# Kernel optimization log

Hardware: AMD Instinct MI355X
Metric: run time of the kernel (lower is better)

The kernel has to match this reference:

```python
import jax, jax.numpy as jnp
import numpy as np
import math

D = 1024
H = 16
HD = D // H
P = 64  # bias_proj_dim
B, N, M = 4, 1024, 2048
EPS_LN = 1e-5
EPS_NORM = 1e-12


def _ln(x, g, b):
    mu = jnp.mean(x, axis=-1, keepdims=True)
    var = jnp.var(x, axis=-1, keepdims=True)
    return (x - mu) * jax.lax.rsqrt(var + EPS_LN) * g + b


def _l2norm_dim1(x):
    # torch F.normalize(x, p=2) default dim=1 -> normalize over the sequence axis
    n = jnp.sqrt(jnp.sum(x * x, axis=1, keepdims=True))
    return x / jnp.maximum(n, EPS_NORM)


def setup_inputs() -> dict:
    key = jax.random.key(0)
    ks = jax.random.split(key, 16)
    s = 1.0 / math.sqrt(D)
    inp = {
        'dataset_features': jax.random.normal(ks[0], (B, N, D), jnp.float32),
        'visual_features': jax.random.normal(ks[1], (B, M, D), jnp.float32),
        # linear weights stored as (in, out): y = x @ W + b
        'wq_w': jax.random.normal(ks[2], (D, D), jnp.float32) * s,
        'wq_b': jnp.zeros((D,), jnp.float32),
        'wk_w': jax.random.normal(ks[3], (D, D), jnp.float32) * s,
        'wk_b': jnp.zeros((D,), jnp.float32),
        'wv_w': jax.random.normal(ks[4], (D, D), jnp.float32) * s,
        'wv_b': jnp.zeros((D,), jnp.float32),
        'wo_w': jax.random.normal(ks[5], (D, D), jnp.float32) * s,
        'wo_b': jnp.zeros((D,), jnp.float32),
        'gq_w': jax.random.normal(ks[6], (D, P), jnp.float32) * s,
        'gq_b': jnp.zeros((P,), jnp.float32),
        'gk_w': jax.random.normal(ks[7], (D, P), jnp.float32) * s,
        'gk_b': jnp.zeros((P,), jnp.float32),
        'pos_scale': jnp.asarray(2.0, jnp.float32),
        'neg_scale': jnp.asarray(50.0, jnp.float32),
        'attn_logit_scale': jnp.asarray(math.log(10.0), jnp.float32),
        'ln_q_g': jnp.ones((D,), jnp.float32),
        'ln_q_b': jnp.zeros((D,), jnp.float32),
        'ln_kv_g': jnp.ones((D,), jnp.float32),
        'ln_kv_b': jnp.zeros((D,), jnp.float32),
        'ln_out_g': jnp.ones((D,), jnp.float32),
        'ln_out_b': jnp.zeros((D,), jnp.float32),
        'ff1_w': jax.random.normal(ks[8], (D, 2 * D), jnp.float32) * s,
        'ff1_b': jnp.zeros((2 * D,), jnp.float32),
        'ff2_w': jax.random.normal(ks[9], (2 * D, D), jnp.float32) * (1.0 / math.sqrt(2 * D)),
        'ff2_b': jnp.zeros((D,), jnp.float32),
    }
    return inp


def reference(dataset_features, visual_features, wq_w, wq_b, wk_w, wk_b, wv_w, wv_b,
              wo_w, wo_b, gq_w, gq_b, gk_w, gk_b, pos_scale, neg_scale,
              attn_logit_scale, ln_q_g, ln_q_b, ln_kv_g, ln_kv_b, ln_out_g, ln_out_b,
              ff1_w, ff1_b, ff2_w, ff2_b):
    residual = dataset_features
    q_in = _ln(dataset_features, ln_q_g, ln_q_b)   # [B,N,D]
    kv_in = _ln(visual_features, ln_kv_g, ln_kv_b)  # [B,M,D]

    geo_q = _l2norm_dim1(q_in @ gq_w + gq_b)   # [B,N,P], normalized over N
    geo_k = _l2norm_dim1(kv_in @ gk_w + gk_b)  # [B,M,P], normalized over M
    bias_raw = jnp.einsum('bnp,bmp->bnm', geo_q, geo_k)  # [B,N,M]
    full_bias = jax.nn.relu(bias_raw) * pos_scale - jax.nn.relu(-bias_raw) * neg_scale

    q = (q_in @ wq_w + wq_b).reshape(B, N, H, HD).transpose(0, 2, 1, 3)   # [B,H,N,hd]
    k = (kv_in @ wk_w + wk_b).reshape(B, M, H, HD).transpose(0, 2, 1, 3)  # [B,H,M,hd]
    v = (kv_in @ wv_w + wv_b).reshape(B, M, H, HD).transpose(0, 2, 1, 3)

    logits = jnp.einsum('bhnd,bhmd->bhnm', q, k) / math.sqrt(HD)
    logits = logits * jnp.exp(attn_logit_scale)
    scores = logits + full_bias[:, None, :, :]
    attn = jax.nn.softmax(scores, axis=-1)
    out = jnp.einsum('bhnm,bhmd->bhnd', attn, v).transpose(0, 2, 1, 3).reshape(B, N, D)
    out = out @ wo_w + wo_b
    out = residual + out

    residual = out
    h = _ln(out, ln_out_g, ln_out_b)
    ff = jax.nn.gelu(h @ ff1_w + ff1_b, approximate=False) @ ff2_w + ff2_b
    return residual + ff
```

## Files before the change

kernel.cpp:

```cpp
#include <hip/hip_runtime.h>


typedef __bf16 bf16x8 __attribute__((ext_vector_type(8)));
typedef float  f32x4  __attribute__((ext_vector_type(4)));

__device__ inline f32x4 mfma16(bf16x8 a, bf16x8 b, f32x4 c) {
  return __builtin_amdgcn_mfma_f32_16x16x32_bf16(a, b, c, 0, 0, 0);
}

__device__ inline void glds16(const void* g, void* l) {
  __builtin_amdgcn_global_load_lds(
      (const __attribute__((address_space(1))) void*)g,
      (__attribute__((address_space(3))) void*)l, 16, 0, 0);
}

#define DB 1024
#define DH 16
#define DHD 64
#define DP 64
#define NB 4
#define NN 1024
#define NM 2048

__global__ __launch_bounds__(256) void k_transpose_all(
    const float* __restrict__ w0, const float* __restrict__ w1,
    const float* __restrict__ w2, const float* __restrict__ w3,
    const float* __restrict__ f1, const float* __restrict__ f2,
    const float* __restrict__ g0, const float* __restrict__ g1,
    __bf16* __restrict__ o0, __bf16* __restrict__ o1,
    __bf16* __restrict__ o2, __bf16* __restrict__ o3,
    __bf16* __restrict__ of1, __bf16* __restrict__ of2,
    __bf16* __restrict__ og0, __bf16* __restrict__ og1) {
  __shared__ float tile[32][33];
  int id = blockIdx.x;
  const float* in;
  __bf16* out;
  int K, O, x, y;
  if (id < 4096) {
    int mi = id >> 10, r = id & 1023;
    in = mi == 0 ? w0 : mi == 1 ? w1 : mi == 2 ? w2 : w3;
    out = mi == 0 ? o0 : mi == 1 ? o1 : mi == 2 ? o2 : o3;
    K = 1024; O = 1024; x = r & 31; y = r >> 5;
  } else if (id < 6144) {
    int r = id - 4096; in = f1; out = of1; K = 1024; O = 2048; x = r & 63; y = r >> 6;
  } else if (id < 8192) {
    int r = id - 6144; in = f2; out = of2; K = 2048; O = 1024; x = r & 31; y = r >> 5;
  } else if (id < 8256) {
    int r = id - 8192; in = g0; out = og0; K = 1024; O = 64; x = r & 1; y = r >> 1;
  } else {
    int r = id - 8256; in = g1; out = og1; K = 1024; O = 64; x = r & 1; y = r >> 1;
  }
  int k0 = y * 32, o0c = x * 32;
  int tx = threadIdx.x & 31, ty = threadIdx.x >> 5;
#pragma unroll
  for (int r = ty; r < 32; r += 8)
    tile[r][tx] = in[(size_t)(k0 + r) * O + (o0c + tx)];
  __syncthreads();
#pragma unroll
  for (int r = ty; r < 32; r += 8)
    out[(size_t)(o0c + r) * K + (k0 + tx)] = (__bf16)tile[tx][r];
}

__device__ inline void ln_body(const float* __restrict__ x,
                               const float* __restrict__ g,
                               const float* __restrict__ bb,
                               __bf16* __restrict__ y, size_t row) {
  int t = threadIdx.x;
  float4 v = ((const float4*)(x + row * 1024))[t];
  float s = v.x + v.y + v.z + v.w;
  float ss = v.x * v.x + v.y * v.y + v.z * v.z + v.w * v.w;
#pragma unroll
  for (int o = 32; o; o >>= 1) {
    s += __shfl_down(s, o, 64);
    ss += __shfl_down(ss, o, 64);
  }
  __shared__ float r1[4], r2[4];
  if ((t & 63) == 0) { r1[t >> 6] = s; r2[t >> 6] = ss; }
  __syncthreads();
  s = r1[0] + r1[1] + r1[2] + r1[3];
  ss = r2[0] + r2[1] + r2[2] + r2[3];
  float mu = s * (1.f / 1024.f);
  float rstd = rsqrtf(ss * (1.f / 1024.f) - mu * mu + 1e-5f);
  float4 gv = ((const float4*)g)[t];
  float4 bv = ((const float4*)bb)[t];
  __bf16* yr = y + row * 1024 + t * 4;
  yr[0] = (__bf16)((v.x - mu) * rstd * gv.x + bv.x);
  yr[1] = (__bf16)((v.y - mu) * rstd * gv.y + bv.y);
  yr[2] = (__bf16)((v.z - mu) * rstd * gv.z + bv.z);
  yr[3] = (__bf16)((v.w - mu) * rstd * gv.w + bv.w);
}

__global__ __launch_bounds__(256) void k_layernorm(
    const float* __restrict__ x, const float* __restrict__ g,
    const float* __restrict__ bb, __bf16* __restrict__ y) {
  ln_body(x, g, bb, y, blockIdx.x);
}

__global__ __launch_bounds__(256) void k_layernorm2(
    const float* __restrict__ x1, const float* __restrict__ g1,
    const float* __restrict__ b1, __bf16* __restrict__ y1,
    const float* __restrict__ x2, const float* __restrict__ g2,
    const float* __restrict__ b2, __bf16* __restrict__ y2) {
  int row = blockIdx.x;
  if (row < 4096) ln_body(x1, g1, b1, y1, row);
  else ln_body(x2, g2, b2, y2, row - 4096);
}

__global__ __launch_bounds__(256) void k_geo(
    const __bf16* __restrict__ qin, const __bf16* __restrict__ kvin,
    const __bf16* __restrict__ gqw, const __bf16* __restrict__ gkw,
    const float* __restrict__ gqb, const float* __restrict__ gkb,
    __bf16* __restrict__ geoq, __bf16* __restrict__ geok) {
  const int blk = blockIdx.x;
  const bool isq = blk < 128;
  const __bf16* A = isq ? qin : kvin;
  const __bf16* Bt = isq ? gqw : gkw;
  const float* bias = isq ? gqb : gkb;
  __bf16* C = isq ? geoq : geok;
  const int row0 = (isq ? blk : blk - 128) * 32;
  __shared__ __align__(16) __bf16 As[32][72], Bs[64][72];
  const int t = threadIdx.x, lane = t & 63, w = t >> 6;
  const int quad = lane >> 4, l15 = lane & 15;
  const int wr = w >> 1, wc = w & 1;
  const int sr = t >> 3, skc = (t & 7) * 8;
  const __bf16* aP = A + (size_t)(row0 + sr) * 1024 + skc;
  const __bf16* bP0 = Bt + (size_t)sr * 1024 + skc;
  const __bf16* bP1 = Bt + (size_t)(sr + 32) * 1024 + skc;
  bf16x8 av = *(const bf16x8*)aP;
  bf16x8 bv0 = *(const bf16x8*)bP0;
  bf16x8 bv1 = *(const bf16x8*)bP1;
  f32x4 acc[2] = {};
  for (int k0 = 0; k0 < 1024; k0 += 64) {
    __syncthreads();
    *(bf16x8*)&As[sr][skc] = av;
    *(bf16x8*)&Bs[sr][skc] = bv0;
    *(bf16x8*)&Bs[sr + 32][skc] = bv1;
    __syncthreads();
    if (k0 + 64 < 1024) {
      av = *(const bf16x8*)(aP + k0 + 64);
      bv0 = *(const bf16x8*)(bP0 + k0 + 64);
      bv1 = *(const bf16x8*)(bP1 + k0 + 64);
    }
#pragma unroll
    for (int ks = 0; ks < 2; ks++) {
      bf16x8 af = *(const bf16x8*)&As[wr * 16 + l15][ks * 32 + quad * 8];
#pragma unroll
      for (int ct = 0; ct < 2; ct++) {
        bf16x8 bfr = *(const bf16x8*)&Bs[wc * 32 + ct * 16 + l15][ks * 32 + quad * 8];
        acc[ct] = mfma16(af, bfr, acc[ct]);
      }
    }
  }
#pragma unroll
  for (int ct = 0; ct < 2; ct++) {
    int col = wc * 32 + ct * 16 + l15;
    float bc = bias[col];
#pragma unroll
    for (int i = 0; i < 4; i++) {
      int row = row0 + wr * 16 + quad * 4 + i;
      C[(size_t)row * 64 + col] = (__bf16)(acc[ct][i] + bc);
    }
  }
}

__global__ __launch_bounds__(256) void k_l2sum(
    const __bf16* __restrict__ gq, const __bf16* __restrict__ gk,
    float* __restrict__ sums) {
  int chunk = blockIdx.x, b = blockIdx.y, z = blockIdx.z;
  if (z == 0 && chunk >= 8) return;
  const __bf16* src = z ? gk : gq;
  int rows = z ? 2048 : 1024;
  const unsigned* base = (const unsigned*)(src + (size_t)b * rows * 64) + chunk * 128 * 32;
  int t = threadIdx.x, c = t & 31, ro = t >> 5;
  float s0 = 0.f, s1 = 0.f;
  for (int r = ro; r < 128; r += 8) {
    unsigned u = base[r * 32 + c];
    float f0 = __uint_as_float(u << 16);
    float f1 = __uint_as_float(u & 0xffff0000u);
    s0 += f0 * f0;
    s1 += f1 * f1;
  }
  __shared__ float ls[64];
  if (t < 64) ls[t] = 0.f;
  __syncthreads();
  atomicAdd(&ls[c * 2], s0);
  atomicAdd(&ls[c * 2 + 1], s1);
  __syncthreads();
  if (t < 64) atomicAdd(&sums[z * 256 + b * 64 + t], ls[t]);
}

__global__ __launch_bounds__(256) void k_l2scale(
    __bf16* __restrict__ gk, const float* __restrict__ sums) {
  int chunk = blockIdx.x, b = blockIdx.y;
  unsigned* base = (unsigned*)(gk + (size_t)b * 2048 * 64) + chunk * 128 * 32;
  int t = threadIdx.x, c = t & 31, ro = t >> 5;
  float sq0 = sums[b * 64 + c * 2], sq1 = sums[b * 64 + c * 2 + 1];
  float sk0 = sums[256 + b * 64 + c * 2], sk1 = sums[256 + b * 64 + c * 2 + 1];
  float m0 = 1.f / (fmaxf(sqrtf(sq0), 1e-12f) * fmaxf(sqrtf(sk0), 1e-12f));
  float m1 = 1.f / (fmaxf(sqrtf(sq1), 1e-12f) * fmaxf(sqrtf(sk1), 1e-12f));
  for (int r = ro; r < 128; r += 8) {
    unsigned u = base[r * 32 + c];
    float f0 = __uint_as_float(u << 16) * m0;
    float f1 = __uint_as_float(u & 0xffff0000u) * m1;
    unsigned short h0 = __builtin_bit_cast(unsigned short, (__bf16)f0);
    unsigned short h1 = __builtin_bit_cast(unsigned short, (__bf16)f1);
    base[r * 32 + c] = (unsigned)h0 | ((unsigned)h1 << 16);
  }
}

__global__ __launch_bounds__(256, 2) void k_qkv(
    const __bf16* __restrict__ qin, const __bf16* __restrict__ kvin,
    const __bf16* __restrict__ twq, const __bf16* __restrict__ twk,
    const __bf16* __restrict__ twv, const float* __restrict__ qbias,
    const float* __restrict__ kbias, const float* __restrict__ vbias,
    __bf16* __restrict__ qb, __bf16* __restrict__ kb, __bf16* __restrict__ vtb) {
  int id = blockIdx.x;
  const __bf16 *A, *Bt;
  const float* bias;
  __bf16* C;
  int my, nx, Ndim;
  bool rowbias;
  if (id < 256) {
    A = qin; Bt = twq; bias = qbias; C = qb;
    nx = id & 7; my = id >> 3; Ndim = 1024; rowbias = false;
  } else if (id < 768) {
    id -= 256;
    A = kvin; Bt = twk; bias = kbias; C = kb;
    nx = id & 7; my = id >> 3; Ndim = 1024; rowbias = false;
  } else {
    id -= 768;
    A = twv; Bt = kvin; bias = vbias; C = vtb;
    nx = id & 63; my = id >> 6; Ndim = 8192; rowbias = true;
  }
  const int Kdim = 1024;
  __shared__ __align__(16) __bf16 As[128 * 32];
  __shared__ __align__(16) __bf16 Bs[128 * 32];
  const int m0 = my * 128, n0 = nx * 128;
  const int t = threadIdx.x, lane = t & 63, w = t >> 6;
  const int quad = lane >> 4, l15 = lane & 15;
  const int wr = w >> 1, wc = w & 1;
  const int srow = lane >> 2, scol = (lane & 3) * 8;
  const __bf16* aS0 = A + (size_t)(m0 + w * 32 + srow) * Kdim + scol;
  const __bf16* bS0 = Bt + (size_t)(n0 + w * 32 + srow) * Kdim + scol;
  const size_t K16 = (size_t)16 * Kdim;
  __bf16* lA0 = &As[(w * 32) * 32];
  __bf16* lB0 = &Bs[(w * 32) * 32];

  f32x4 acc[4][4] = {};
  for (int k0 = 0; k0 < Kdim; k0 += 32) {
    __syncthreads();
    glds16(aS0 + k0, lA0);
    glds16(aS0 + K16 + k0, lA0 + 16 * 32);
    glds16(bS0 + k0, lB0);
    glds16(bS0 + K16 + k0, lB0 + 16 * 32);
    __syncthreads();
    bf16x8 af[4], bg[4];
#pragma unroll
    for (int rt = 0; rt < 4; rt++)
      af[rt] = *(const bf16x8*)&As[(wr * 64 + rt * 16 + l15) * 32 + quad * 8];
#pragma unroll
    for (int ct = 0; ct < 4; ct++)
      bg[ct] = *(const bf16x8*)&Bs[(wc * 64 + ct * 16 + l15) * 32 + quad * 8];
#pragma unroll
    for (int rt = 0; rt < 4; rt++)
#pragma unroll
      for (int ct = 0; ct < 4; ct++)
        acc[rt][ct] = mfma16(af[rt], bg[ct], acc[rt][ct]);
  }
#pragma unroll
  for (int rt = 0; rt < 4; rt++) {
    int row = m0 + wr * 64 + rt * 16 + quad * 4;
#pragma unroll
    for (int ct = 0; ct < 4; ct++) {
      int col = n0 + wc * 64 + ct * 16 + l15;
      float bcol = rowbias ? 0.f : bias[col];
#pragma unroll
      for (int i = 0; i < 4; i++) {
        float vv = acc[rt][ct][i] + (rowbias ? bias[row + i] : bcol);
        C[(size_t)(row + i) * Ndim + col] = (__bf16)vv;
      }
    }
  }
}

template <int EPI>
__global__ __launch_bounds__(256, 2) void k_gemm128(
    const __bf16* __restrict__ A, const __bf16* __restrict__ Bt,
    const float* __restrict__ bias, const float* __restrict__ resid,
    void* __restrict__ Cout, int Mdim, int Ndim, int Kdim) {
  __shared__ __align__(16) __bf16 As[128 * 32];
  __shared__ __align__(16) __bf16 Bs[128 * 32];
  const int m0 = blockIdx.y * 128, n0 = blockIdx.x * 128;
  const int t = threadIdx.x, lane = t & 63, w = t >> 6;
  const int quad = lane >> 4, l15 = lane & 15;
  const int wr = w >> 1, wc = w & 1;
  const int srow = lane >> 2, scol = (lane & 3) * 8;
  const __bf16* aS0 = A + (size_t)(m0 + w * 32 + srow) * Kdim + scol;
  const __bf16* bS0 = Bt + (size_t)(n0 + w * 32 + srow) * Kdim + scol;
  const size_t K16 = (size_t)16 * Kdim;
  __bf16* lA0 = &As[(w * 32) * 32];
  __bf16* lB0 = &Bs[(w * 32) * 32];

  f32x4 acc[4][4] = {};
  for (int k0 = 0; k0 < Kdim; k0 += 32) {
    __syncthreads();
    glds16(aS0 + k0, lA0);
    glds16(aS0 + K16 + k0, lA0 + 16 * 32);
    glds16(bS0 + k0, lB0);
    glds16(bS0 + K16 + k0, lB0 + 16 * 32);
    __syncthreads();
    bf16x8 af[4], bg[4];
#pragma unroll
    for (int rt = 0; rt < 4; rt++)
      af[rt] = *(const bf16x8*)&As[(wr * 64 + rt * 16 + l15) * 32 + quad * 8];
#pragma unroll
    for (int ct = 0; ct < 4; ct++)
      bg[ct] = *(const bf16x8*)&Bs[(wc * 64 + ct * 16 + l15) * 32 + quad * 8];
#pragma unroll
    for (int rt = 0; rt < 4; rt++)
#pragma unroll
      for (int ct = 0; ct < 4; ct++)
        acc[rt][ct] = mfma16(af[rt], bg[ct], acc[rt][ct]);
  }
#pragma unroll
  for (int rt = 0; rt < 4; rt++) {
    int row = m0 + wr * 64 + rt * 16 + quad * 4;
#pragma unroll
    for (int ct = 0; ct < 4; ct++) {
      int col = n0 + wc * 64 + ct * 16 + l15;
      float bcol = bias[col];
#pragma unroll
      for (int i = 0; i < 4; i++) {
        float vv = acc[rt][ct][i] + bcol;
        size_t idx = (size_t)(row + i) * Ndim + col;
        if (EPI == 2) {
          ((float*)Cout)[idx] = vv + resid[idx];
        } else {
          ((__bf16*)Cout)[idx] = (__bf16)(0.5f * vv * (1.f + erff(vv * 0.70710678118f)));
        }
      }
    }
  }
}

__global__ __launch_bounds__(256, 2) void k_flash(
    const __bf16* __restrict__ Q, const __bf16* __restrict__ K,
    const __bf16* __restrict__ Vt, const __bf16* __restrict__ Gq,
    const __bf16* __restrict__ Gk, const float* __restrict__ als,
    const float* __restrict__ psc, const float* __restrict__ nsc,
    __bf16* __restrict__ Out) {
  const int o = blockIdx.x;
  const int bh = o & 63, x = o >> 6;
  const int b = bh & 3, h = bh >> 2;
  const int t = threadIdx.x, w = t >> 6, lane = t & 63;
  const int quad = lane >> 4, l15 = lane & 15;
  const int row0 = x * 128 + w * 32;
  const float sc = __expf(als[0]) * 0.125f;
  const float pos = psc[0], neg = nsc[0];

  __shared__ __align__(16) __bf16 Ks[64][72];
  __shared__ __align__(16) __bf16 Gs[64][72];
  __shared__ __align__(16) __bf16 Vs[64][72];
  __shared__ __align__(16) __bf16 plds[4][32][72];

  const __bf16* Qb = Q + ((size_t)(b * NN + row0)) * DB + h * DHD;
  const __bf16* Kb = K + ((size_t)b * NM) * DB + h * DHD;
  const __bf16* Vb = Vt + (size_t)(h * DHD) * (NB * NM) + (size_t)b * NM;
  const __bf16* Gqb = Gq + (size_t)(b * NN + row0) * DP;
  const __bf16* Gkb = Gk + (size_t)b * NM * DP;

  const int r0 = t >> 3, c0 = (t & 7) * 8;
  const int r1 = r0 + 32;

  bf16x8 qf[2][2], gqf[2][2];
#pragma unroll
  for (int rt = 0; rt < 2; rt++)
#pragma unroll
    for (int ks = 0; ks < 2; ks++) {
      qf[rt][ks] = *(const bf16x8*)(Qb + (size_t)(rt * 16 + l15) * DB + ks * 32 + quad * 8);
      gqf[rt][ks] = *(const bf16x8*)(Gqb + (size_t)(rt * 16 + l15) * DP + ks * 32 + quad * 8);
    }

  bf16x8 kst0 = *(const bf16x8*)(Kb + (size_t)r0 * DB + c0);
  bf16x8 kst1 = *(const bf16x8*)(Kb + (size_t)r1 * DB + c0);
  bf16x8 gst0 = *(const bf16x8*)(Gkb + (size_t)r0 * DP + c0);
  bf16x8 gst1 = *(const bf16x8*)(Gkb + (size_t)r1 * DP + c0);
  bf16x8 vst0 = *(const bf16x8*)(Vb + (size_t)r0 * (NB * NM) + c0);
  bf16x8 vst1 = *(const bf16x8*)(Vb + (size_t)r1 * (NB * NM) + c0);

  float lrow[2][4] = {};
  f32x4 oacc[2][4] = {};
  f32x4 z4 = {0.f, 0.f, 0.f, 0.f};

  for (int m0 = 0; m0 < NM; m0 += 64) {
    __syncthreads();
    *(bf16x8*)&Ks[r0][c0] = kst0;
    *(bf16x8*)&Ks[r1][c0] = kst1;
    *(bf16x8*)&Gs[r0][c0] = gst0;
    *(bf16x8*)&Gs[r1][c0] = gst1;
    *(bf16x8*)&Vs[r0][c0] = vst0;
    *(bf16x8*)&Vs[r1][c0] = vst1;
    __syncthreads();
    if (m0 + 64 < NM) {
      kst0 = *(const bf16x8*)(Kb + (size_t)(m0 + 64 + r0) * DB + c0);
      kst1 = *(const bf16x8*)(Kb + (size_t)(m0 + 64 + r1) * DB + c0);
      gst0 = *(const bf16x8*)(Gkb + (size_t)(m0 + 64 + r0) * DP + c0);
      gst1 = *(const bf16x8*)(Gkb + (size_t)(m0 + 64 + r1) * DP + c0);
      vst0 = *(const bf16x8*)(Vb + (size_t)r0 * (NB * NM) + m0 + 64 + c0);
      vst1 = *(const bf16x8*)(Vb + (size_t)r1 * (NB * NM) + m0 + 64 + c0);
    }
    bf16x8 kf[4][2], gkf[4][2];
#pragma unroll
    for (int ct = 0; ct < 4; ct++)
#pragma unroll
      for (int ks = 0; ks < 2; ks++) {
        kf[ct][ks] = *(const bf16x8*)&Ks[ct * 16 + l15][ks * 32 + quad * 8];
        gkf[ct][ks] = *(const bf16x8*)&Gs[ct * 16 + l15][ks * 32 + quad * 8];
      }
#pragma unroll
    for (int rt = 0; rt < 2; rt++)
#pragma unroll
      for (int ct = 0; ct < 4; ct++) {
        f32x4 s = mfma16(qf[rt][1], kf[ct][1], mfma16(qf[rt][0], kf[ct][0], z4));
        f32x4 bg = mfma16(gqf[rt][1], gkf[ct][1], mfma16(gqf[rt][0], gkf[ct][0], z4));
#pragma unroll
        for (int i = 0; i < 4; i++) {
          float bb = bg[i];
          float fb = bb > 0.f ? bb * pos : bb * neg;
          float p = __expf(s[i] * sc + fb);
          lrow[rt][i] += p;
          plds[w][rt * 16 + quad * 4 + i][ct * 16 + l15] = (__bf16)p;
        }
      }
    bf16x8 pf[2][2], vf[4][2];
#pragma unroll
    for (int rt = 0; rt < 2; rt++)
#pragma unroll
      for (int ms = 0; ms < 2; ms++)
        pf[rt][ms] = *(const bf16x8*)&plds[w][rt * 16 + l15][ms * 32 + quad * 8];
#pragma unroll
    for (int dt = 0; dt < 4; dt++)
#pragma unroll
      for (int ms = 0; ms < 2; ms++)
        vf[dt][ms] = *(const bf16x8*)&Vs[dt * 16 + l15][ms * 32 + quad * 8];
#pragma unroll
    for (int rt = 0; rt < 2; rt++)
#pragma unroll
      for (int dt = 0; dt < 4; dt++) {
        oacc[rt][dt] = mfma16(pf[rt][0], vf[dt][0], oacc[rt][dt]);
        oacc[rt][dt] = mfma16(pf[rt][1], vf[dt][1], oacc[rt][dt]);
      }
  }
#pragma unroll
  for (int rt = 0; rt < 2; rt++)
#pragma unroll
    for (int i = 0; i < 4; i++) {
      float l = lrow[rt][i];
#pragma unroll
      for (int o2 = 1; o2 < 16; o2 <<= 1) l += __shfl_xor(l, o2, 64);
      float inv = 1.f / l;
#pragma unroll
      for (int dt = 0; dt < 4; dt++)
        Out[(size_t)(b * NN + row0 + rt * 16 + quad * 4 + i) * DB + h * DHD + dt * 16 + l15] =
            (__bf16)(oacc[rt][dt][i] * inv);
    }
}

extern "C" void kernel_launch(void* const* d_in, const int* in_sizes, int n_in,
                              void* d_out, int out_size, void* d_ws, size_t ws_size,
                              hipStream_t stream) {
  const float* dataset = (const float*)d_in[0];
  const float* visual = (const float*)d_in[1];
  const float* wq_w = (const float*)d_in[2];
  const float* wq_b = (const float*)d_in[3];
  const float* wk_w = (const float*)d_in[4];
  const float* wk_b = (const float*)d_in[5];
  const float* wv_w = (const float*)d_in[6];
  const float* wv_b = (const float*)d_in[7];
  const float* wo_w = (const float*)d_in[8];
  const float* wo_b = (const float*)d_in[9];
  const float* gq_w = (const float*)d_in[10];
  const float* gq_b = (const float*)d_in[11];
  const float* gk_w = (const float*)d_in[12];
  const float* gk_b = (const float*)d_in[13];
  const float* pos_scale = (const float*)d_in[14];
  const float* neg_scale = (const float*)d_in[15];
  const float* als = (const float*)d_in[16];
  const float* ln_q_g = (const float*)d_in[17];
  const float* ln_q_b = (const float*)d_in[18];
  const float* ln_kv_g = (const float*)d_in[19];
  const float* ln_kv_b = (const float*)d_in[20];
  const float* ln_out_g = (const float*)d_in[21];
  const float* ln_out_b = (const float*)d_in[22];
  const float* ff1_w = (const float*)d_in[23];
  const float* ff1_b = (const float*)d_in[24];
  const float* ff2_w = (const float*)d_in[25];
  const float* ff2_b = (const float*)d_in[26];

  char* ws = (char*)d_ws;
  size_t off = 0;
  auto alloc = [&](size_t bytes) {
    size_t o = off;
    off += (bytes + 255) & ~(size_t)255;
    return o;
  };
  __bf16* t_wq = (__bf16*)(ws + alloc((size_t)1024 * 1024 * 2));
  __bf16* t_wk = (__bf16*)(ws + alloc((size_t)1024 * 1024 * 2));
  __bf16* t_wv = (__bf16*)(ws + alloc((size_t)1024 * 1024 * 2));
  __bf16* t_wo = (__bf16*)(ws + alloc((size_t)1024 * 1024 * 2));
  __bf16* t_ff1 = (__bf16*)(ws + alloc((size_t)2048 * 1024 * 2));
  __bf16* t_ff2 = (__bf16*)(ws + alloc((size_t)1024 * 2048 * 2));
  __bf16* t_gq = (__bf16*)(ws + alloc((size_t)64 * 1024 * 2));
  __bf16* t_gk = (__bf16*)(ws + alloc((size_t)64 * 1024 * 2));
  size_t qin_off = alloc((size_t)4096 * 1024 * 2);
  size_t kvin_off = alloc((size_t)8192 * 1024 * 2);
  __bf16* qin = (__bf16*)(ws + qin_off);
  __bf16* kvin = (__bf16*)(ws + kvin_off);
  __bf16* geoq = (__bf16*)(ws + alloc((size_t)4096 * 64 * 2));
  __bf16* geok = (__bf16*)(ws + alloc((size_t)8192 * 64 * 2));
  float* sums = (float*)(ws + alloc((size_t)2 * 4 * 64 * 4));
  __bf16* qb = (__bf16*)(ws + alloc((size_t)4096 * 1024 * 2));
  __bf16* kb = (__bf16*)(ws + alloc((size_t)8192 * 1024 * 2));
  __bf16* vtb = (__bf16*)(ws + alloc((size_t)1024 * 8192 * 2));
  __bf16* attn = (__bf16*)(ws + alloc((size_t)4096 * 1024 * 2));
  __bf16* ffh = (__bf16*)(ws + alloc((size_t)4096 * 2048 * 2));
  float* out1 = (float*)(ws + kvin_off);
  __bf16* hbuf = (__bf16*)(ws + qin_off);
  float* outp = (float*)d_out;

  dim3 blk(256);
  k_transpose_all<<<8320, blk, 0, stream>>>(wq_w, wk_w, wv_w, wo_w, ff1_w, ff2_w,
                                            gq_w, gk_w, t_wq, t_wk, t_wv, t_wo,
                                            t_ff1, t_ff2, t_gq, t_gk);
  k_layernorm2<<<12288, blk, 0, stream>>>(dataset, ln_q_g, ln_q_b, qin,
                                          visual, ln_kv_g, ln_kv_b, kvin);
  k_geo<<<384, blk, 0, stream>>>(qin, kvin, t_gq, t_gk, gq_b, gk_b, geoq, geok);
  hipMemsetAsync(sums, 0, 2 * 4 * 64 * 4, stream);
  k_l2sum<<<dim3(16, 4, 2), blk, 0, stream>>>(geoq, geok, sums);
  k_l2scale<<<dim3(16, 4), blk, 0, stream>>>(geok, sums);
  k_qkv<<<1280, blk, 0, stream>>>(qin, kvin, t_wq, t_wk, t_wv,
                                  wq_b, wk_b, wv_b, qb, kb, vtb);
  k_flash<<<512, blk, 0, stream>>>(qb, kb, vtb, geoq, geok, als,
                                   pos_scale, neg_scale, attn);
  k_gemm128<2><<<dim3(8, 32), blk, 0, stream>>>(attn, t_wo, wo_b, dataset, out1,
                                                4096, 1024, 1024);
  k_layernorm<<<4096, blk, 0, stream>>>(out1, ln_out_g, ln_out_b, hbuf);
  k_gemm128<3><<<dim3(16, 32), blk, 0, stream>>>(hbuf, t_ff1, ff1_b, nullptr, ffh,
                                                 4096, 2048, 1024);
  k_gemm128<2><<<dim3(8, 32), blk, 0, stream>>>(ffh, t_ff2, ff2_b, out1, outp,
                                                4096, 1024, 2048);
}
```

Baseline: 456.0 us.

## Split flash attention over KV halves, swizzle LDS, use narrower output GEMMs

The flash kernel now splits the 2048-key range into two halves, which doubles the grid to 1024 blocks. Each half writes unnormalized fp32 partial outputs and row sums, and a new combine kernel merges them into bf16. The flash kernel also switches its LDS tiles to an XOR-swizzled unpadded layout and folds the softmax scales into a single exp2 with fmaf. The N=1024 output GEMMs use a new 128x64 tile kernel so more blocks fill the GPU, and the GELU GEMM and QKV kernel raise their occupancy hint to 3. The cost is extra fp32 partial traffic and one more kernel launch.

After: 458.9 us. No clear change (+0.6%).

```diff
diff --git a/kernel.cpp b/kernel.cpp
--- a/kernel.cpp
+++ b/kernel.cpp
@@ -12,6 +12,10 @@
   __builtin_amdgcn_global_load_lds(
       (const __attribute__((address_space(1))) void*)g,
       (__attribute__((address_space(3))) void*)l, 16, 0, 0);
+}
+
+__device__ inline int swz(int row, int col) {
+  return row * 64 + ((((col >> 3) ^ (row & 7)) << 3) | (col & 7));
 }
 
 #define DB 1024
@@ -208,7 +212,7 @@
   }
 }
 
-__global__ __launch_bounds__(256, 2) void k_qkv(
+__global__ __launch_bounds__(256, 3) void k_qkv(
     const __bf16* __restrict__ qin, const __bf16* __restrict__ kvin,
     const __bf16* __restrict__ twq, const __bf16* __restrict__ twk,
     const __bf16* __restrict__ twv, const float* __restrict__ qbias,
@@ -283,11 +287,10 @@
   }
 }
 
-template <int EPI>
-__global__ __launch_bounds__(256, 2) void k_gemm128(
+__global__ __launch_bounds__(256, 3) void k_gemm128g(
     const __bf16* __restrict__ A, const __bf16* __restrict__ Bt,
-    const float* __restrict__ bias, const float* __restrict__ resid,
-    void* __restrict__ Cout, int Mdim, int Ndim, int Kdim) {
+    const float* __restrict__ bias, __bf16* __restrict__ Cout,
+    int Ndim, int Kdim) {
   __shared__ __align__(16) __bf16 As[128 * 32];
   __shared__ __align__(16) __bf16 Bs[128 * 32];
   const int m0 = blockIdx.y * 128, n0 = blockIdx.x * 128;
@@ -332,12 +335,61 @@
 #pragma unroll
       for (int i = 0; i < 4; i++) {
         float vv = acc[rt][ct][i] + bcol;
+        Cout[(size_t)(row + i) * Ndim + col] =
+            (__bf16)(0.5f * vv * (1.f + erff(vv * 0.70710678118f)));
+      }
+    }
+  }
+}
+
+__global__ __launch_bounds__(256, 2) void k_gemmn64(
+    const __bf16* __restrict__ A, const __bf16* __restrict__ Bt,
+    const float* __restrict__ bias, const float* __restrict__ resid,
+    float* __restrict__ Cout, int Ndim, int Kdim) {
+  __shared__ __align__(16) __bf16 As[128 * 32];
+  __shared__ __align__(16) __bf16 Bs[64 * 32];
+  const int m0 = blockIdx.y * 128, n0 = blockIdx.x * 64;
+  const int t = threadIdx.x, lane = t & 63, w = t >> 6;
+  const int quad = lane >> 4, l15 = lane & 15;
+  const int wr = w >> 1, wc = w & 1;
+  const int srow = lane >> 2, scol = (lane & 3) * 8;
+  const __bf16* aS0 = A + (size_t)(m0 + w * 32 + srow) * Kdim + scol;
+  const __bf16* bS0 = Bt + (size_t)(n0 + w * 16 + srow) * Kdim + scol;
+  const size_t K16 = (size_t)16 * Kdim;
+  __bf16* lA0 = &As[(w * 32) * 32];
+  __bf16* lB0 = &Bs[(w * 16) * 32];
+
+  f32x4 acc[4][2] = {};
+  for (int k0 = 0; k0 < Kdim; k0 += 32) {
+    __syncthreads();
+    glds16(aS0 + k0, lA0);
+    glds16(aS0 + K16 + k0, lA0 + 16 * 32);
+    glds16(bS0 + k0, lB0);
+    __syncthreads();
+    bf16x8 af[4], bg[2];
+#pragma unroll
+    for (int rt = 0; rt < 4; rt++)
+      af[rt] = *(const bf16x8*)&As[(wr * 64 + rt * 16 + l15) * 32 + quad * 8];
+#pragma unroll
+    for (int ct = 0; ct < 2; ct++)
+      bg[ct] = *(const bf16x8*)&Bs[(wc * 32 + ct * 16 + l15) * 32 + quad * 8];
+#pragma unroll
+    for (int rt = 0; rt < 4; rt++)
+#pragma unroll
+      for (int ct = 0; ct < 2; ct++)
+        acc[rt][ct] = mfma16(af[rt], bg[ct], acc[rt][ct]);
+  }
+#pragma unroll
+  for (int rt = 0; rt < 4; rt++) {
+    int row = m0 + wr * 64 + rt * 16 + quad * 4;
+#pragma unroll
+    for (int ct = 0; ct < 2; ct++) {
+      int col = n0 + wc * 32 + ct * 16 + l15;
+      float bcol = bias[col];
+#pragma unroll
+      for (int i = 0; i < 4; i++) {
         size_t idx = (size_t)(row + i) * Ndim + col;
-        if (EPI == 2) {
-          ((float*)Cout)[idx] = vv + resid[idx];
-        } else {
-          ((__bf16*)Cout)[idx] = (__bf16)(0.5f * vv * (1.f + erff(vv * 0.70710678118f)));
-        }
+        Cout[idx] = acc[rt][ct][i] + bcol + resid[idx];
       }
     }
   }
@@ -348,20 +400,21 @@
     const __bf16* __restrict__ Vt, const __bf16* __restrict__ Gq,
     const __bf16* __restrict__ Gk, const float* __restrict__ als,
     const float* __restrict__ psc, const float* __restrict__ nsc,
-    __bf16* __restrict__ Out) {
+    float* __restrict__ Opart, float* __restrict__ lpart) {
   const int o = blockIdx.x;
-  const int bh = o & 63, x = o >> 6;
+  const int bh = o & 63, kv = (o >> 6) & 1, x = o >> 7;
   const int b = bh & 3, h = bh >> 2;
   const int t = threadIdx.x, w = t >> 6, lane = t & 63;
   const int quad = lane >> 4, l15 = lane & 15;
   const int row0 = x * 128 + w * 32;
-  const float sc = __expf(als[0]) * 0.125f;
-  const float pos = psc[0], neg = nsc[0];
-
-  __shared__ __align__(16) __bf16 Ks[64][72];
-  __shared__ __align__(16) __bf16 Gs[64][72];
-  __shared__ __align__(16) __bf16 Vs[64][72];
-  __shared__ __align__(16) __bf16 plds[4][32][72];
+  const float LOG2E = 1.44269504089f;
+  const float sc2 = __expf(als[0]) * 0.125f * LOG2E;
+  const float pos2 = psc[0] * LOG2E, neg2 = nsc[0] * LOG2E;
+
+  __shared__ __align__(16) __bf16 Ks[64 * 64];
+  __shared__ __align__(16) __bf16 Gs[64 * 64];
+  __shared__ __align__(16) __bf16 Vs[64 * 64];
+  __shared__ __align__(16) __bf16 plds[4][32 * 64];
 
   const __bf16* Qb = Q + ((size_t)(b * NN + row0)) * DB + h * DHD;
   const __bf16* Kb = K + ((size_t)b * NM) * DB + h * DHD;
@@ -369,7 +422,8 @@
   const __bf16* Gqb = Gq + (size_t)(b * NN + row0) * DP;
   const __bf16* Gkb = Gk + (size_t)b * NM * DP;
 
-  const int r0 = t >> 3, c0 = (t & 7) * 8;
+  const int r0 = t >> 3, ch = t & 7, gc = ch * 8;
+  const int sw0 = swz(r0, gc), sw1 = sw0 + 32 * 64;
   const int r1 = r0 + 32;
 
   bf16x8 qf[2][2], gqf[2][2];
@@ -381,41 +435,43 @@
       gqf[rt][ks] = *(const bf16x8*)(Gqb + (size_t)(rt * 16 + l15) * DP + ks * 32 + quad * 8);
     }
 
-  bf16x8 kst0 = *(const bf16x8*)(Kb + (size_t)r0 * DB + c0);
-  bf16x8 kst1 = *(const bf16x8*)(Kb + (size_t)r1 * DB + c0);
-  bf16x8 gst0 = *(const bf16x8*)(Gkb + (size_t)r0 * DP + c0);
-  bf16x8 gst1 = *(const bf16x8*)(Gkb + (size_t)r1 * DP + c0);
-  bf16x8 vst0 = *(const bf16x8*)(Vb + (size_t)r0 * (NB * NM) + c0);
-  bf16x8 vst1 = *(const bf16x8*)(Vb + (size_t)r1 * (NB * NM) + c0);
+  const int mlo = kv * 1024;
+  bf16x8 kst0 = *(const bf16x8*)(Kb + (size_t)(mlo + r0) * DB + gc);
+  bf16x8 kst1 = *(const bf16x8*)(Kb + (size_t)(mlo + r1) * DB + gc);
+  bf16x8 gst0 = *(const bf16x8*)(Gkb + (size_t)(mlo + r0) * DP + gc);
+  bf16x8 gst1 = *(const bf16x8*)(Gkb + (size_t)(mlo + r1) * DP + gc);
+  bf16x8 vst0 = *(const bf16x8*)(Vb + (size_t)r0 * (NB * NM) + mlo + gc);
+  bf16x8 vst1 = *(const bf16x8*)(Vb + (size_t)r1 * (NB * NM) + mlo + gc);
 
   float lrow[2][4] = {};
   f32x4 oacc[2][4] = {};
   f32x4 z4 = {0.f, 0.f, 0.f, 0.f};
 
-  for (int m0 = 0; m0 < NM; m0 += 64) {
-    __syncthreads();
-    *(bf16x8*)&Ks[r0][c0] = kst0;
-    *(bf16x8*)&Ks[r1][c0] = kst1;
-    *(bf16x8*)&Gs[r0][c0] = gst0;
-    *(bf16x8*)&Gs[r1][c0] = gst1;
-    *(bf16x8*)&Vs[r0][c0] = vst0;
-    *(bf16x8*)&Vs[r1][c0] = vst1;
-    __syncthreads();
-    if (m0 + 64 < NM) {
-      kst0 = *(const bf16x8*)(Kb + (size_t)(m0 + 64 + r0) * DB + c0);
-      kst1 = *(const bf16x8*)(Kb + (size_t)(m0 + 64 + r1) * DB + c0);
-      gst0 = *(const bf16x8*)(Gkb + (size_t)(m0 + 64 + r0) * DP + c0);
-      gst1 = *(const bf16x8*)(Gkb + (size_t)(m0 + 64 + r1) * DP + c0);
-      vst0 = *(const bf16x8*)(Vb + (size_t)r0 * (NB * NM) + m0 + 64 + c0);
-      vst1 = *(const bf16x8*)(Vb + (size_t)r1 * (NB * NM) + m0 + 64 + c0);
+  for (int m0 = mlo; m0 < mlo + 1024; m0 += 64) {
+    __syncthreads();
+    *(bf16x8*)&Ks[sw0] = kst0;
+    *(bf16x8*)&Ks[sw1] = kst1;
+    *(bf16x8*)&Gs[sw0] = gst0;
+    *(bf16x8*)&Gs[sw1] = gst1;
+    *(bf16x8*)&Vs[sw0] = vst0;
+    *(bf16x8*)&Vs[sw1] = vst1;
+    __syncthreads();
+    if (m0 + 64 < mlo + 1024) {
+      kst0 = *(const bf16x8*)(Kb + (size_t)(m0 + 64 + r0) * DB + gc);
+      kst1 = *(const bf16x8*)(Kb + (size_t)(m0 + 64 + r1) * DB + gc);
+      gst0 = *(const bf16x8*)(Gkb + (size_t)(m0 + 64 + r0) * DP + gc);
+      gst1 = *(const bf16x8*)(Gkb + (size_t)(m0 + 64 + r1) * DP + gc);
+      vst0 = *(const bf16x8*)(Vb + (size_t)r0 * (NB * NM) + m0 + 64 + gc);
+      vst1 = *(const bf16x8*)(Vb + (size_t)r1 * (NB * NM) + m0 + 64 + gc);
     }
     bf16x8 kf[4][2], gkf[4][2];
 #pragma unroll
     for (int ct = 0; ct < 4; ct++)
 #pragma unroll
       for (int ks = 0; ks < 2; ks++) {
-        kf[ct][ks] = *(const bf16x8*)&Ks[ct * 16 + l15][ks * 32 + quad * 8];
-        gkf[ct][ks] = *(const bf16x8*)&Gs[ct * 16 + l15][ks * 32 + quad * 8];
+        int off = swz(ct * 16 + l15, ks * 32 + quad * 8);
+        kf[ct][ks] = *(const bf16x8*)&Ks[off];
+        gkf[ct][ks] = *(const bf16x8*)&Gs[off];
       }
 #pragma unroll
     for (int rt = 0; rt < 2; rt++)
@@ -426,10 +482,10 @@
 #pragma unroll
         for (int i = 0; i < 4; i++) {
           float bb = bg[i];
-          float fb = bb > 0.f ? bb * pos : bb * neg;
-          float p = __expf(s[i] * sc + fb);
+          float scl = bb > 0.f ? pos2 : neg2;
+          float p = __builtin_amdgcn_exp2f(fmaf(bb, scl, s[i] * sc2));
           lrow[rt][i] += p;
-          plds[w][rt * 16 + quad * 4 + i][ct * 16 + l15] = (__bf16)p;
+          plds[w][swz(rt * 16 + quad * 4 + i, ct * 16 + l15)] = (__bf16)p;
         }
       }
     bf16x8 pf[2][2], vf[4][2];
@@ -437,12 +493,12 @@
     for (int rt = 0; rt < 2; rt++)
 #pragma unroll
       for (int ms = 0; ms < 2; ms++)
-        pf[rt][ms] = *(const bf16x8*)&plds[w][rt * 16 + l15][ms * 32 + quad * 8];
+        pf[rt][ms] = *(const bf16x8*)&plds[w][swz(rt * 16 + l15, ms * 32 + quad * 8)];
 #pragma unroll
     for (int dt = 0; dt < 4; dt++)
 #pragma unroll
       for (int ms = 0; ms < 2; ms++)
-        vf[dt][ms] = *(const bf16x8*)&Vs[dt * 16 + l15][ms * 32 + quad * 8];
+        vf[dt][ms] = *(const bf16x8*)&Vs[swz(dt * 16 + l15, ms * 32 + quad * 8)];
 #pragma unroll
     for (int rt = 0; rt < 2; rt++)
 #pragma unroll
@@ -451,6 +507,8 @@
         oacc[rt][dt] = mfma16(pf[rt][1], vf[dt][1], oacc[rt][dt]);
       }
   }
+  float* op = Opart + ((size_t)kv * NB * NN + b * NN + row0) * DB + h * 64;
+  float* lp = lpart + ((size_t)kv * NB * NN + b * NN + row0) * DH + h;
 #pragma unroll
   for (int rt = 0; rt < 2; rt++)
 #pragma unroll
@@ -458,12 +516,29 @@
       float l = lrow[rt][i];
 #pragma unroll
       for (int o2 = 1; o2 < 16; o2 <<= 1) l += __shfl_xor(l, o2, 64);
-      float inv = 1.f / l;
+      int r = rt * 16 + quad * 4 + i;
 #pragma unroll
       for (int dt = 0; dt < 4; dt++)
-        Out[(size_t)(b * NN + row0 + rt * 16 + quad * 4 + i) * DB + h * DHD + dt * 16 + l15] =
-            (__bf16)(oacc[rt][dt][i] * inv);
-    }
+        op[(size_t)r * DB + dt * 16 + l15] = oacc[rt][dt][i];
+      if (l15 == 0) lp[(size_t)r * DH] = l;
+    }
+}
+
+__global__ __launch_bounds__(256) void k_combine(
+    const float* __restrict__ Opart, const float* __restrict__ lpart,
+    __bf16* __restrict__ attn) {
+  const int bn = blockIdx.x;
+  const int t = threadIdx.x, c = t * 4, h = c >> 6;
+  const float4 o0 = *(const float4*)&Opart[(size_t)bn * DB + c];
+  const float4 o1 = *(const float4*)&Opart[((size_t)NB * NN + bn) * DB + c];
+  float l0 = lpart[(size_t)bn * DH + h];
+  float l1 = lpart[((size_t)NB * NN + bn) * DH + h];
+  float inv = 1.f / (l0 + l1);
+  __bf16* dst = attn + (size_t)bn * DB + c;
+  dst[0] = (__bf16)((o0.x + o1.x) * inv);
+  dst[1] = (__bf16)((o0.y + o1.y) * inv);
+  dst[2] = (__bf16)((o0.z + o1.z) * inv);
+  dst[3] = (__bf16)((o0.w + o1.w) * inv);
 }
 
 extern "C" void kernel_launch(void* const* d_in, const int* in_sizes, int n_in,
@@ -524,6 +599,8 @@
   __bf16* vtb = (__bf16*)(ws + alloc((size_t)1024 * 8192 * 2));
   __bf16* attn = (__bf16*)(ws + alloc((size_t)4096 * 1024 * 2));
   __bf16* ffh = (__bf16*)(ws + alloc((size_t)4096 * 2048 * 2));
+  float* opart = (float*)(ws + alloc((size_t)2 * 4096 * 1024 * 4));
+  float* lpart = (float*)(ws + alloc((size_t)2 * 4096 * 16 * 4));
   float* out1 = (float*)(ws + kvin_off);
   __bf16* hbuf = (__bf16*)(ws + qin_off);
   float* outp = (float*)d_out;
@@ -540,13 +617,14 @@
   k_l2scale<<<dim3(16, 4), blk, 0, stream>>>(geok, sums);
   k_qkv<<<1280, blk, 0, stream>>>(qin, kvin, t_wq, t_wk, t_wv,
                                   wq_b, wk_b, wv_b, qb, kb, vtb);
-  k_flash<<<512, blk, 0, stream>>>(qb, kb, vtb, geoq, geok, als,
-                                   pos_scale, neg_scale, attn);
-  k_gemm128<2><<<dim3(8, 32), blk, 0, stream>>>(attn, t_wo, wo_b, dataset, out1,
-                                                4096, 1024, 1024);
+  k_flash<<<1024, blk, 0, stream>>>(qb, kb, vtb, geoq, geok, als,
+                                    pos_scale, neg_scale, opart, lpart);
+  k_combine<<<4096, blk, 0, stream>>>(opart, lpart, attn);
+  k_gemmn64<<<dim3(16, 32), blk, 0, stream>>>(attn, t_wo, wo_b, dataset, out1,
+                                              1024, 1024);
   k_layernorm<<<4096, blk, 0, stream>>>(out1, ln_out_g, ln_out_b, hbuf);
-  k_gemm128<3><<<dim3(16, 32), blk, 0, stream>>>(hbuf, t_ff1, ff1_b, nullptr, ffh,
-                                                 4096, 2048, 1024);
-  k_gemm128<2><<<dim3(8, 32), blk, 0, stream>>>(ffh, t_ff2, ff2_b, out1, outp,
-                                                4096, 1024, 2048);
-}
+  k_gemm128g<<<dim3(16, 32), blk, 0, stream>>>(hbuf, t_ff1, ff1_b, ffh,
+                                               2048, 1024);
+  k_gemmn64<<<dim3(16, 32), blk, 0, stream>>>(ffh, t_ff2, ff2_b, out1, outp,
+                                              1024, 2048);
+}
```
